# Kernel optimization log

Measured on AMD Instinct MI355X. Metric: run time of the kernel, lower is better.

## Reference

```python
import jax, jax.numpy as jnp
import numpy as np

N_NODES = 50000
N_EDGES = 400000
D_IN = 64
D_HID = 64
D_OUT = 64
NEG_SLOPE = 0.2   # GATConv LeakyReLU slope
BN_EPS = 1e-5


def _add_self_loops(row, col, N):
    loop = jnp.arange(N, dtype=row.dtype)
    return jnp.concatenate([row, loop]), jnp.concatenate([col, loop])


def _gcn_conv(x, row, col, N, W, b):
    # PyG GCNConv: add self loops, symmetric normalization, sum aggregate, bias
    r, c = _add_self_loops(row, col, N)
    deg = jax.ops.segment_sum(jnp.ones_like(r, dtype=x.dtype), c, num_segments=N)
    dis = jnp.where(deg > 0, deg ** -0.5, 0.0)
    norm = dis[r] * dis[c]                       # [E+N]
    h = x @ W                                    # [N, out]
    out = jax.ops.segment_sum(h[r] * norm[:, None], c, num_segments=N)
    return out + b


def _gat_conv(x, row, col, N, W, att_src, att_dst, b, concat):
    # PyG GATConv: per-edge attention with softmax over incoming edges
    H, C = att_src.shape
    r, c = _add_self_loops(row, col, N)
    h = (x @ W).reshape(N, H, C)
    a_src = jnp.einsum('nhc,hc->nh', h, att_src)
    a_dst = jnp.einsum('nhc,hc->nh', h, att_dst)
    e = jax.nn.leaky_relu(a_src[r] + a_dst[c], NEG_SLOPE)   # [E', H]
    m = jax.ops.segment_max(e, c, num_segments=N)           # stable softmax per target
    e = jnp.exp(e - m[c])
    denom = jax.ops.segment_sum(e, c, num_segments=N)
    alpha = e / denom[c]                                    # [E', H]
    out = jax.ops.segment_sum(h[r] * alpha[:, :, None], c, num_segments=N)  # [N,H,C]
    out = out.reshape(N, H * C) if concat else out.mean(axis=1)
    return out + b


def _sage_conv(x, row, col, N, Wl, bl, Wr):
    # PyG SAGEConv(aggr='mean', normalize=True): lin_l(mean_j x_j) + lin_r(x), then L2-normalize
    s = jax.ops.segment_sum(x[row], col, num_segments=N)
    cnt = jax.ops.segment_sum(jnp.ones_like(row, dtype=x.dtype), col, num_segments=N)
    mean = s / jnp.maximum(cnt, 1.0)[:, None]
    out = mean @ Wl + bl + x @ Wr
    n = jnp.linalg.norm(out, axis=-1, keepdims=True)
    return out / jnp.maximum(n, 1e-12)


def _forward(x, edge_index, gate_w1, gate_b1, gate_w2, gate_b2,
             gcn_w1, gcn_b1, bn_gamma, bn_beta, gcn_w2, gcn_b2,
             gat_w1, gat_att_src1, gat_att_dst1, gat_b1,
             gat_w2, gat_att_src2, gat_att_dst2, gat_b2,
             sage_wl1, sage_bl1, sage_wr1, sage_wl2, sage_bl2, sage_wr2):
    N = x.shape[0]
    row, col = edge_index[0], edge_index[1]
    # gate: mean node feature -> MLP -> softmax over 3 models
    g = jnp.mean(x, axis=0, keepdims=True)
    w = jax.nn.softmax(jax.nn.relu(g @ gate_w1 + gate_b1) @ gate_w2 + gate_b2, axis=-1)
    # GCN branch (eval: BatchNorm with running mean=0, var=1; dropout off)
    h = _gcn_conv(x, row, col, N, gcn_w1, gcn_b1)
    h = h * (bn_gamma / jnp.sqrt(1.0 + BN_EPS)) + bn_beta
    h = jax.nn.relu(h)
    out_gcn = _gcn_conv(h, row, col, N, gcn_w2, gcn_b2)
    # GAT branch: hidden layer 4 heads concat + ELU, output layer 1 head mean
    h = jax.nn.elu(_gat_conv(x, row, col, N, gat_w1, gat_att_src1, gat_att_dst1, gat_b1, True))
    out_gat = _gat_conv(h, row, col, N, gat_w2, gat_att_src2, gat_att_dst2, gat_b2, False)
    # SAGE branch
    h = jax.nn.relu(_sage_conv(x, row, col, N, sage_wl1, sage_bl1, sage_wr1))
    out_sage = _sage_conv(h, row, col, N, sage_wl2, sage_bl2, sage_wr2)
    return w[0, 0] * out_gcn + w[0, 1] * out_gat + w[0, 2] * out_sage


def setup_inputs() -> dict:
    key = jax.random.key(0)
    ks = jax.random.split(key, 16)
    def nrm(k, shape, scale=0.05):
        return jax.random.normal(k, shape, dtype=jnp.float32) * scale
    inp = {}
    inp['x'] = jax.random.normal(ks[0], (N_NODES, D_IN), dtype=jnp.float32)
    inp['edge_index'] = jax.random.randint(ks[1], (2, N_EDGES), 0, N_NODES, dtype=jnp.int32)
    inp['gate_w1'] = nrm(ks[2], (D_IN, 64)); inp['gate_b1'] = jnp.zeros((64,), jnp.float32)
    inp['gate_w2'] = nrm(ks[3], (64, 3));    inp['gate_b2'] = jnp.zeros((3,), jnp.float32)
    inp['gcn_w1'] = nrm(ks[4], (D_IN, D_HID)); inp['gcn_b1'] = jnp.zeros((D_HID,), jnp.float32)
    inp['bn_gamma'] = jnp.ones((D_HID,), jnp.float32); inp['bn_beta'] = jnp.zeros((D_HID,), jnp.float32)
    inp['gcn_w2'] = nrm(ks[5], (D_HID, D_OUT)); inp['gcn_b2'] = jnp.zeros((D_OUT,), jnp.float32)
    inp['gat_w1'] = nrm(ks[6], (D_IN, 4 * D_HID))
    inp['gat_att_src1'] = nrm(ks[7], (4, D_HID)); inp['gat_att_dst1'] = nrm(ks[8], (4, D_HID))
    inp['gat_b1'] = jnp.zeros((4 * D_HID,), jnp.float32)
    inp['gat_w2'] = nrm(ks[9], (4 * D_HID, D_OUT))
    inp['gat_att_src2'] = nrm(ks[10], (1, D_OUT)); inp['gat_att_dst2'] = nrm(ks[11], (1, D_OUT))
    inp['gat_b2'] = jnp.zeros((D_OUT,), jnp.float32)
    inp['sage_wl1'] = nrm(ks[12], (D_IN, D_HID)); inp['sage_bl1'] = jnp.zeros((D_HID,), jnp.float32)
    inp['sage_wr1'] = nrm(ks[13], (D_IN, D_HID))
    inp['sage_wl2'] = nrm(ks[14], (D_HID, D_OUT)); inp['sage_bl2'] = jnp.zeros((D_OUT,), jnp.float32)
    inp['sage_wr2'] = nrm(ks[15], (D_HID, D_OUT))
    return inp


def reference(x, edge_index, gate_w1, gate_b1, gate_w2, gate_b2,
              gcn_w1, gcn_b1, bn_gamma, bn_beta, gcn_w2, gcn_b2,
              gat_w1, gat_att_src1, gat_att_dst1, gat_b1,
              gat_w2, gat_att_src2, gat_att_dst2, gat_b2,
              sage_wl1, sage_bl1, sage_wr1, sage_wl2, sage_bl2, sage_wr2):
    return _forward(x, edge_index, gate_w1, gate_b1, gate_w2, gate_b2,
                    gcn_w1, gcn_b1, bn_gamma, bn_beta, gcn_w2, gcn_b2,
                    gat_w1, gat_att_src1, gat_att_dst1, gat_b1,
                    gat_w2, gat_att_src2, gat_att_dst2, gat_b2,
                    sage_wl1, sage_bl1, sage_wr1, sage_wl2, sage_bl2, sage_wr2)
```

## Files before the change

### kernel.cpp

```cpp
#include <hip/hip_runtime.h>
#include <hip/hip_bf16.h>
#include <math.h>

#define NN 50000
#define NE 400000

typedef __attribute__((ext_vector_type(8))) short bf16x8;
typedef __attribute__((ext_vector_type(4))) float f32x4;

__device__ __forceinline__ float lrelu(float v){ return v > 0.f ? v : 0.2f*v; }
__device__ __forceinline__ float elu1(float v){ return v > 0.f ? v : expm1f(v); }
__device__ __forceinline__ float bflo(unsigned int u){ return __uint_as_float(u << 16); }
__device__ __forceinline__ float bfhi(unsigned int u){ return __uint_as_float(u & 0xffff0000u); }
__device__ __forceinline__ unsigned short f2bf(float f){
  __hip_bfloat16 h = __float2bfloat16(f);
  return *(unsigned short*)&h;
}
__device__ __forceinline__ unsigned int pack2(float lo, float hi){
  return (unsigned int)f2bf(lo) | ((unsigned int)f2bf(hi) << 16);
}

__device__ __forceinline__ void stage_tab(unsigned short* Wt, const unsigned short* Wb, int tid){
  #pragma unroll
  for(int s = 0; s < 2; s++){
    int c = tid + s*256;
    int n = c >> 3, ko = (c & 7)*8;
    *(bf16x8*)&Wt[n*72 + ko] = *(const bf16x8*)&Wb[n*64 + ko];
  }
}

__global__ void k_count(const int* __restrict__ col, int* __restrict__ cnt, int E){
  int e = blockIdx.x*blockDim.x + threadIdx.x;
  if(e < E) atomicAdd(&cnt[col[e]], 1);
}

__global__ void k_alloc(const int* __restrict__ cnt, int* __restrict__ offs,
                        float* __restrict__ dis, float* __restrict__ invc,
                        int* __restrict__ total, int N){
  int i = blockIdx.x*blockDim.x + threadIdx.x;
  int lane = threadIdx.x & 63;
  int v = (i < N) ? cnt[i] : 0;
  int x = v;
  #pragma unroll
  for(int d = 1; d < 64; d <<= 1){ int t = __shfl_up(x, d, 64); if(lane >= d) x += t; }
  int base = 0;
  if(lane == 63 && x > 0) base = atomicAdd(total, x);
  base = __shfl(base, 63, 64);
  if(i < N){
    offs[i] = base + x - v;
    dis[i]  = 1.0f / sqrtf((float)(v + 1));
    invc[i] = 1.0f / fmaxf((float)v, 1.0f);
  }
}

__global__ void k_fill(const int* __restrict__ row, const int* __restrict__ col,
                       const int* __restrict__ offs, int* __restrict__ cursor,
                       int* __restrict__ csr, int E){
  int e = blockIdx.x*blockDim.x + threadIdx.x;
  if(e < E){
    int c = col[e];
    int pos = offs[c] + atomicAdd(&cursor[c], 1);
    csr[pos] = row[e];
  }
}

struct PKS { const float* src; unsigned short* dst; int kshift; int ldw; int col0; };
struct PKP { PKS s[11]; };

__global__ void k_packw(PKP p){
  PKS s = p.s[blockIdx.x];
  int K = 1 << s.kshift;
  int total = K << 6;
  for(int idx = threadIdx.x; idx < total; idx += 256){
    int n = idx >> s.kshift, k = idx & (K - 1);
    s.dst[idx] = f2bf(s.src[(size_t)k*s.ldw + s.col0 + n]);
  }
}

__global__ void k_castsum(const float* __restrict__ x, unsigned short* __restrict__ xb,
                          float* __restrict__ gsum, int N){
  __shared__ float part[4][64];
  int lane = threadIdx.x & 63, w = threadIdx.x >> 6;
  float s = 0.f;
  for(int r = blockIdx.x*4 + w; r < N; r += gridDim.x*4){
    float v = x[(size_t)r*64 + lane];
    xb[(size_t)r*64 + lane] = f2bf(v);
    s += v;
  }
  part[w][lane] = s;
  __syncthreads();
  if(w == 0) atomicAdd(&gsum[lane], part[0][lane]+part[1][lane]+part[2][lane]+part[3][lane]);
}

__global__ void k_gate(const float* __restrict__ gsum,
                       const float* __restrict__ w1, const float* __restrict__ b1,
                       const float* __restrict__ w2, const float* __restrict__ b2,
                       float* __restrict__ gatew){
  __shared__ float g[64]; __shared__ float hid[64]; __shared__ float lg[3];
  int t = threadIdx.x;
  g[t] = gsum[t] * (1.0f/(float)NN);
  __syncthreads();
  float acc = b1[t];
  for(int i = 0; i < 64; i++) acc += g[i]*w1[i*64 + t];
  hid[t] = fmaxf(acc, 0.f);
  __syncthreads();
  if(t < 3){
    float a = b2[t];
    for(int j = 0; j < 64; j++) a += hid[j]*w2[j*3 + t];
    lg[t] = a;
  }
  __syncthreads();
  if(t == 0){
    float m = fmaxf(lg[0], fmaxf(lg[1], lg[2]));
    float e0 = expf(lg[0]-m), e1 = expf(lg[1]-m), e2 = expf(lg[2]-m);
    float s = e0 + e1 + e2;
    gatew[0] = e0/s; gatew[1] = e1/s; gatew[2] = e2/s;
  }
}

__global__ void k_fold1(const float* __restrict__ w1, const float* __restrict__ as,
                        const float* __restrict__ ad, float* __restrict__ wsd){
  int t = threadIdx.x;
  int k = t & 63, h = t >> 6;
  float ssrc = 0.f, sdst = 0.f;
  for(int c = 0; c < 64; c++){
    float w = w1[k*256 + h*64 + c];
    ssrc += w * as[h*64 + c];
    sdst += w * ad[h*64 + c];
  }
  wsd[k*8 + h] = ssrc;
  wsd[k*8 + 4 + h] = sdst;
}

__global__ void k_attdotx(const unsigned short* __restrict__ xb, const float* __restrict__ wsd,
                          float* __restrict__ asrc, float* __restrict__ adst, int N){
  __shared__ float ws[64*8];
  int tid = threadIdx.x;
  ws[tid] = wsd[tid];
  ws[tid + 256] = wsd[tid + 256];
  __syncthreads();
  int node = blockIdx.x*16 + (tid >> 4);
  int l = tid & 15;
  if(node >= N) return;
  uint2 u = *(const uint2*)&xb[(size_t)node*64 + l*4];
  float v0 = bflo(u.x), v1 = bfhi(u.x), v2 = bflo(u.y), v3 = bfhi(u.y);
  float s[8];
  #pragma unroll
  for(int h = 0; h < 8; h++){
    s[h] = v0*ws[(l*4+0)*8+h] + v1*ws[(l*4+1)*8+h] + v2*ws[(l*4+2)*8+h] + v3*ws[(l*4+3)*8+h];
  }
  #pragma unroll
  for(int d = 8; d >= 1; d >>= 1){
    #pragma unroll
    for(int h = 0; h < 8; h++) s[h] += __shfl_xor(s[h], d, 16);
  }
  if(l == 0){
    float4 o1; o1.x = s[0]; o1.y = s[1]; o1.z = s[2]; o1.w = s[3];
    float4 o2; o2.x = s[4]; o2.y = s[5]; o2.z = s[6]; o2.w = s[7];
    *(float4*)&asrc[node*4] = o1;
    *(float4*)&adst[node*4] = o2;
  }
}

__global__ void k_edgew1(const float* __restrict__ asrc, const float* __restrict__ adst,
                         const int* __restrict__ offs, const int* __restrict__ cnt,
                         const int* __restrict__ csr,
                         float* __restrict__ wvE, float* __restrict__ rdenN,
                         float* __restrict__ wvS, int N){
  int node = blockIdx.x*4 + (threadIdx.x >> 6);
  int lane = threadIdx.x & 63;
  if(node >= N) return;
  float4 ad = *(const float4*)&adst[node*4];
  float a0 = 0.f, a1 = 0.f, a2 = 0.f, a3 = 0.f;
  int e0 = offs[node], e1 = e0 + cnt[node];
  for(int e = e0 + lane; e < e1; e += 64){
    int s = csr[e];
    float4 as = *(const float4*)&asrc[s*4];
    float4 w;
    w.x = expf(lrelu(as.x + ad.x));
    w.y = expf(lrelu(as.y + ad.y));
    w.z = expf(lrelu(as.z + ad.z));
    w.w = expf(lrelu(as.w + ad.w));
    a0 += w.x; a1 += w.y; a2 += w.z; a3 += w.w;
    *(float4*)&wvE[(size_t)e*4] = w;
  }
  #pragma unroll
  for(int d = 32; d >= 1; d >>= 1){
    a0 += __shfl_xor(a0, d, 64); a1 += __shfl_xor(a1, d, 64);
    a2 += __shfl_xor(a2, d, 64); a3 += __shfl_xor(a3, d, 64);
  }
  float4 asl = *(const float4*)&asrc[node*4];
  float4 ws;
  ws.x = expf(lrelu(asl.x + ad.x));
  ws.y = expf(lrelu(asl.y + ad.y));
  ws.z = expf(lrelu(asl.z + ad.z));
  ws.w = expf(lrelu(asl.w + ad.w));
  if(lane == 0){
    float4 rd;
    rd.x = 1.0f/(a0 + ws.x); rd.y = 1.0f/(a1 + ws.y);
    rd.z = 1.0f/(a2 + ws.z); rd.w = 1.0f/(a3 + ws.w);
    *(float4*)&rdenN[node*4] = rd;
    *(float4*)&wvS[node*4] = ws;
  }
}

__global__ void k_edgew2(const float* __restrict__ asrc, const float* __restrict__ adst,
                         const int* __restrict__ offs, const int* __restrict__ cnt,
                         const int* __restrict__ csr,
                         float* __restrict__ wvE, float* __restrict__ rdenN,
                         float* __restrict__ wvS, int N){
  int node = blockIdx.x*4 + (threadIdx.x >> 6);
  int lane = threadIdx.x & 63;
  if(node >= N) return;
  float ad = adst[node];
  float acc = 0.f;
  int e0 = offs[node], e1 = e0 + cnt[node];
  for(int e = e0 + lane; e < e1; e += 64){
    float w = expf(lrelu(asrc[csr[e]] + ad));
    acc += w;
    wvE[e] = w;
  }
  #pragma unroll
  for(int d = 32; d >= 1; d >>= 1) acc += __shfl_xor(acc, d, 64);
  float ws = expf(lrelu(asrc[node] + ad));
  if(lane == 0){
    rdenN[node] = 1.0f/(acc + ws);
    wvS[node] = ws;
  }
}

__global__ void k_aggx(const unsigned short* __restrict__ xb,
                       const float* __restrict__ wvE, const float* __restrict__ rden,
                       const float* __restrict__ wvS,
                       const float* __restrict__ dis, const float* __restrict__ invc,
                       const int* __restrict__ offs, const int* __restrict__ cnt,
                       const int* __restrict__ csr,
                       unsigned short* __restrict__ z, unsigned short* __restrict__ agcnx,
                       unsigned short* __restrict__ asagex, int N){
  int node = blockIdx.x*4 + (threadIdx.x >> 6);
  int lane = threadIdx.x & 63;
  if(node >= N) return;
  int half = lane >> 5, subl = lane & 31;
  float zg[4][2] = {{0,0},{0,0},{0,0},{0,0}};
  float gg[2] = {0,0}, ssv[2] = {0,0};
  int e0 = offs[node], e1 = e0 + cnt[node];
  #pragma unroll 2
  for(int e = e0 + half; e < e1; e += 2){
    int s = csr[e];
    float4 w4 = *(const float4*)&wvE[(size_t)e*4];
    float ds = dis[s];
    unsigned int u = *(const unsigned int*)&xb[(size_t)s*64 + subl*2];
    float xl = bflo(u), xh = bfhi(u);
    zg[0][0] = fmaf(w4.x, xl, zg[0][0]); zg[0][1] = fmaf(w4.x, xh, zg[0][1]);
    zg[1][0] = fmaf(w4.y, xl, zg[1][0]); zg[1][1] = fmaf(w4.y, xh, zg[1][1]);
    zg[2][0] = fmaf(w4.z, xl, zg[2][0]); zg[2][1] = fmaf(w4.z, xh, zg[2][1]);
    zg[3][0] = fmaf(w4.w, xl, zg[3][0]); zg[3][1] = fmaf(w4.w, xh, zg[3][1]);
    gg[0] = fmaf(ds, xl, gg[0]); gg[1] = fmaf(ds, xh, gg[1]);
    ssv[0] += xl; ssv[1] += xh;
  }
  #pragma unroll
  for(int h = 0; h < 4; h++){
    zg[h][0] += __shfl_xor(zg[h][0], 32, 64);
    zg[h][1] += __shfl_xor(zg[h][1], 32, 64);
  }
  gg[0] += __shfl_xor(gg[0], 32, 64); gg[1] += __shfl_xor(gg[1], 32, 64);
  ssv[0] += __shfl_xor(ssv[0], 32, 64); ssv[1] += __shfl_xor(ssv[1], 32, 64);
  if(half == 0){
    unsigned int un = *(const unsigned int*)&xb[(size_t)node*64 + subl*2];
    float xl = bflo(un), xh = bfhi(un);
    float4 ws4 = *(const float4*)&wvS[node*4];
    float4 rd4 = *(const float4*)&rden[node*4];
    unsigned int* zp = (unsigned int*)&z[(size_t)node*256 + subl*2];
    zp[0]   = pack2((zg[0][0] + ws4.x*xl)*rd4.x, (zg[0][1] + ws4.x*xh)*rd4.x);
    zp[32]  = pack2((zg[1][0] + ws4.y*xl)*rd4.y, (zg[1][1] + ws4.y*xh)*rd4.y);
    zp[64]  = pack2((zg[2][0] + ws4.z*xl)*rd4.z, (zg[2][1] + ws4.z*xh)*rd4.z);
    zp[96]  = pack2((zg[3][0] + ws4.w*xl)*rd4.w, (zg[3][1] + ws4.w*xh)*rd4.w);
    float dc = dis[node], ic = invc[node];
    *(unsigned int*)&agcnx[(size_t)node*64 + subl*2] =
        pack2(dc*fmaf(dc, xl, gg[0]), dc*fmaf(dc, xh, gg[1]));
    *(unsigned int*)&asagex[(size_t)node*64 + subl*2] = pack2(ssv[0]*ic, ssv[1]*ic);
  }
}

__global__ void k_aggf(const unsigned short* __restrict__ a1, const unsigned short* __restrict__ s1,
                       const unsigned short* __restrict__ h2,
                       const float* __restrict__ wvE, const float* __restrict__ rden,
                       const float* __restrict__ wvS,
                       const float* __restrict__ dis, const float* __restrict__ invc,
                       const int* __restrict__ offs, const int* __restrict__ cnt,
                       const int* __restrict__ csr,
                       unsigned short* __restrict__ A2agg, unsigned short* __restrict__ S2agg,
                       unsigned short* __restrict__ T2, int N){
  int node = blockIdx.x*4 + (threadIdx.x >> 6);
  int lane = threadIdx.x & 63;
  if(node >= N) return;
  int half = lane >> 5, subl = lane & 31;
  float aa[2] = {0,0}, ss[2] = {0,0}, tt[2] = {0,0};
  int e0 = offs[node], e1 = e0 + cnt[node];
  #pragma unroll 2
  for(int e = e0 + half; e < e1; e += 2){
    int s = csr[e];
    float ds = dis[s];
    float wv = wvE[e];
    unsigned int ua = *(const unsigned int*)&a1[(size_t)s*64 + subl*2];
    unsigned int us = *(const unsigned int*)&s1[(size_t)s*64 + subl*2];
    unsigned int uh = *(const unsigned int*)&h2[(size_t)s*64 + subl*2];
    aa[0] = fmaf(ds, bflo(ua), aa[0]); aa[1] = fmaf(ds, bfhi(ua), aa[1]);
    ss[0] += bflo(us); ss[1] += bfhi(us);
    tt[0] = fmaf(wv, bflo(uh), tt[0]); tt[1] = fmaf(wv, bfhi(uh), tt[1]);
  }
  aa[0] += __shfl_xor(aa[0], 32, 64); aa[1] += __shfl_xor(aa[1], 32, 64);
  ss[0] += __shfl_xor(ss[0], 32, 64); ss[1] += __shfl_xor(ss[1], 32, 64);
  tt[0] += __shfl_xor(tt[0], 32, 64); tt[1] += __shfl_xor(tt[1], 32, 64);
  if(half == 0){
    unsigned int uan = *(const unsigned int*)&a1[(size_t)node*64 + subl*2];
    unsigned int uhn = *(const unsigned int*)&h2[(size_t)node*64 + subl*2];
    float dc = dis[node], ic = invc[node];
    float rd = rden[node], wss = wvS[node];
    *(unsigned int*)&A2agg[(size_t)node*64 + subl*2] =
        pack2(dc*fmaf(dc, bflo(uan), aa[0]), dc*fmaf(dc, bfhi(uan), aa[1]));
    *(unsigned int*)&S2agg[(size_t)node*64 + subl*2] = pack2(ss[0]*ic, ss[1]*ic);
    *(unsigned int*)&T2[(size_t)node*64 + subl*2] =
        pack2(fmaf(wss, bflo(uhn), tt[0])*rd, fmaf(wss, bfhi(uhn), tt[1])*rd);
  }
}

struct MME {
  const unsigned short* A; const unsigned short* Wb;
  const unsigned short* A2; const unsigned short* Wb2;
  unsigned short* C;
  const float* b; const float* p1; const float* p2;
  int ep;
};
struct FSP {
  const unsigned short* z; const unsigned short* wb1; const float* b1;
  const unsigned short* wb2; const float* as2; const float* ad2;
  unsigned short* h2; float* asrc2; float* adst2;
  MME mm[2];
  int N;
};

__global__ __launch_bounds__(256, 4) void k_fused1(FSP p){
  __shared__ unsigned short smem[16896];
  const int N = p.N;
  int tid = threadIdx.x;
  int w = tid >> 6, lane = tid & 63, quad = lane >> 4, m16 = lane & 15;
  int rowa = blockIdx.x*64 + w*16 + m16;
  int rowc = rowa < N ? rowa : N - 1;
  int robase = blockIdx.x*64 + w*16 + quad*4;

  if(blockIdx.y == 0){
    unsigned short* GH = smem;
    int lr = w*16;
    #pragma unroll
    for(int h = 0; h < 4; h++){
      bf16x8 a0 = *(const bf16x8*)&p.z[(size_t)rowc*256 + h*64 + quad*8];
      bf16x8 a1 = *(const bf16x8*)&p.z[(size_t)rowc*256 + h*64 + 32 + quad*8];
      f32x4 acc[4];
      #pragma unroll
      for(int t = 0; t < 4; t++){ acc[t][0]=0.f; acc[t][1]=0.f; acc[t][2]=0.f; acc[t][3]=0.f; }
      #pragma unroll
      for(int t = 0; t < 4; t++){
        const unsigned short* wb = p.wb1 + (size_t)h*4096 + (t*16 + m16)*64;
        bf16x8 b0 = *(const bf16x8*)&wb[quad*8];
        bf16x8 b1v = *(const bf16x8*)&wb[32 + quad*8];
        acc[t] = __builtin_amdgcn_mfma_f32_16x16x32_bf16(a0, b0, acc[t], 0, 0, 0);
        acc[t] = __builtin_amdgcn_mfma_f32_16x16x32_bf16(a1, b1v, acc[t], 0, 0, 0);
      }
      #pragma unroll
      for(int t = 0; t < 4; t++){
        float bv = p.b1[h*64 + t*16 + m16];
        #pragma unroll
        for(int r = 0; r < 4; r++){
          GH[(lr + quad*4 + r)*264 + h*64 + t*16 + m16] = f2bf(elu1(acc[t][r] + bv));
        }
      }
    }
    __syncthreads();
    f32x4 acc2[4];
    #pragma unroll
    for(int t = 0; t < 4; t++){ acc2[t][0]=0.f; acc2[t][1]=0.f; acc2[t][2]=0.f; acc2[t][3]=0.f; }
    #pragma unroll
    for(int kc = 0; kc < 256; kc += 64){
      bf16x8 a0 = *(const bf16x8*)&GH[(lr + m16)*264 + kc + quad*8];
      bf16x8 a1 = *(const bf16x8*)&GH[(lr + m16)*264 + kc + 32 + quad*8];
      #pragma unroll
      for(int t = 0; t < 4; t++){
        const unsigned short* wb = p.wb2 + (size_t)(t*16 + m16)*256 + kc;
        bf16x8 b0 = *(const bf16x8*)&wb[quad*8];
        bf16x8 b1v = *(const bf16x8*)&wb[32 + quad*8];
        acc2[t] = __builtin_amdgcn_mfma_f32_16x16x32_bf16(a0, b0, acc2[t], 0, 0, 0);
        acc2[t] = __builtin_amdgcn_mfma_f32_16x16x32_bf16(a1, b1v, acc2[t], 0, 0, 0);
      }
    }
    #pragma unroll
    for(int t = 0; t < 4; t++){
      int col = t*16 + m16;
      #pragma unroll
      for(int r = 0; r < 4; r++){
        int ro = robase + r;
        if(ro < N) p.h2[(size_t)ro*64 + col] = f2bf(acc2[t][r]);
      }
    }
    float ps[4] = {0,0,0,0}, pd[4] = {0,0,0,0};
    #pragma unroll
// ... 151 lines not shown
  }
  float w0 = gatew[0], w1 = gatew[1], w2 = gatew[2];
  int robase = blockIdx.x*64 + w*16 + quad*4;
  float vs[4][4], n2[4] = {0,0,0,0};
  #pragma unroll
  for(int t = 0; t < 4; t++){
    float bsv = bl2[t*16 + m16];
    #pragma unroll
    for(int r = 0; r < 4; r++){ vs[t][r] = accs[t][r] + bsv; n2[r] = fmaf(vs[t][r], vs[t][r], n2[r]); }
  }
  #pragma unroll
  for(int d = 8; d >= 1; d >>= 1){
    #pragma unroll
    for(int r = 0; r < 4; r++) n2[r] += __shfl_xor(n2[r], d, 64);
  }
  float inv[4];
  #pragma unroll
  for(int r = 0; r < 4; r++) inv[r] = 1.0f / fmaxf(sqrtf(n2[r]), 1e-12f);
  #pragma unroll
  for(int t = 0; t < 4; t++){
    int col = t*16 + m16;
    float bg = gcn_b2[col], bt = gat_b2[col];
    #pragma unroll
    for(int r = 0; r < 4; r++){
      int ro = robase + r;
      if(ro < N){
        float t2 = bflo((unsigned int)T2[(size_t)ro*64 + col]);
        out[(size_t)ro*64 + col] = w0*(accg[t][r] + bg) + w1*(t2 + bt) + w2*vs[t][r]*inv[r];
      }
    }
  }
}

extern "C" void kernel_launch(void* const* d_in, const int* in_sizes, int n_in,
                              void* d_out, int out_size, void* d_ws, size_t ws_size,
                              hipStream_t stream){
  const float* x        = (const float*)d_in[0];
  const int*   ei       = (const int*)d_in[1];
  const int*   row      = ei;
  const int*   col      = ei + NE;
  const float* gate_w1  = (const float*)d_in[2];
  const float* gate_b1  = (const float*)d_in[3];
  const float* gate_w2  = (const float*)d_in[4];
  const float* gate_b2  = (const float*)d_in[5];
  const float* gcn_w1   = (const float*)d_in[6];
  const float* gcn_b1   = (const float*)d_in[7];
  const float* bn_gamma = (const float*)d_in[8];
  const float* bn_beta  = (const float*)d_in[9];
  const float* gcn_w2   = (const float*)d_in[10];
  const float* gcn_b2   = (const float*)d_in[11];
  const float* gat_w1   = (const float*)d_in[12];
  const float* gat_as1  = (const float*)d_in[13];
  const float* gat_ad1  = (const float*)d_in[14];
  const float* gat_b1   = (const float*)d_in[15];
  const float* gat_w2   = (const float*)d_in[16];
  const float* gat_as2  = (const float*)d_in[17];
  const float* gat_ad2  = (const float*)d_in[18];
  const float* gat_b2   = (const float*)d_in[19];
  const float* sage_wl1 = (const float*)d_in[20];
  const float* sage_bl1 = (const float*)d_in[21];
  const float* sage_wr1 = (const float*)d_in[22];
  const float* sage_wl2 = (const float*)d_in[23];
  const float* sage_bl2 = (const float*)d_in[24];
  const float* sage_wr2 = (const float*)d_in[25];
  float* out = (float*)d_out;

  char* wp = (char*)d_ws;
  auto alloc = [&](size_t bytes)->char*{ char* p = wp; wp += (bytes + 255) & ~(size_t)255; return p; };
  int*   cnt    = (int*)  alloc((size_t)NN*4);
  int*   cursor = (int*)  alloc((size_t)NN*4);
  float* gsum   = (float*)alloc(64*4);
  int*   total  = (int*)  alloc(256);
  size_t zbytes = (size_t)(wp - (char*)cnt);
  int*   offs   = (int*)  alloc((size_t)NN*4);
  int*   csr    = (int*)  alloc((size_t)NE*4);
  float* dis    = (float*)alloc((size_t)NN*4);
  float* invc   = (float*)alloc((size_t)NN*4);
  float* gatew  = (float*)alloc(16);
  float* wsd    = (float*)alloc(64*8*4);
  float* asrc1  = (float*)alloc((size_t)NN*4*4);
  float* adst1  = (float*)alloc((size_t)NN*4*4);
  float* asrc2  = (float*)alloc((size_t)NN*4);
  float* adst2  = (float*)alloc((size_t)NN*4);
  float* wvE1   = (float*)alloc((size_t)NE*4*4);
  float* rden1  = (float*)alloc((size_t)NN*4*4);
  float* wvS1   = (float*)alloc((size_t)NN*4*4);
  float* wvE2   = (float*)alloc((size_t)NE*4);
  float* rden2  = (float*)alloc((size_t)NN*4);
  float* wvS2   = (float*)alloc((size_t)NN*4);
  unsigned short* xb     = (unsigned short*)alloc((size_t)NN*64*2);
  unsigned short* z      = (unsigned short*)alloc((size_t)NN*256*2);
  unsigned short* agcnx  = (unsigned short*)alloc((size_t)NN*64*2);
  unsigned short* asagex = (unsigned short*)alloc((size_t)NN*64*2);
  unsigned short* a1     = (unsigned short*)alloc((size_t)NN*64*2);
  unsigned short* s1     = (unsigned short*)alloc((size_t)NN*64*2);
  unsigned short* h2     = (unsigned short*)alloc((size_t)NN*64*2);
  unsigned short* A2agg  = (unsigned short*)alloc((size_t)NN*64*2);
  unsigned short* S2agg  = (unsigned short*)alloc((size_t)NN*64*2);
  unsigned short* T2     = (unsigned short*)alloc((size_t)NN*64*2);
  unsigned short* wb_gcn1 = (unsigned short*)alloc((size_t)64*64*2);
  unsigned short* wb_wl1  = (unsigned short*)alloc((size_t)64*64*2);
  unsigned short* wb_wr1  = (unsigned short*)alloc((size_t)64*64*2);
  unsigned short* wb_gat1 = (unsigned short*)alloc((size_t)256*64*2);
  unsigned short* wb_gat2 = (unsigned short*)alloc((size_t)64*256*2);
  unsigned short* wb_gcn2 = (unsigned short*)alloc((size_t)64*64*2);
  unsigned short* wb_wl2  = (unsigned short*)alloc((size_t)64*64*2);
  unsigned short* wb_wr2  = (unsigned short*)alloc((size_t)64*64*2);

  hipMemsetAsync(cnt, 0, zbytes, stream);

  const int gN  = (NN + 63) / 64;
  const int g4  = NN / 4;
  const int g16 = NN / 16;
  const int gA  = (NN + 255) / 256;

  {
    PKP pk = {};
    pk.s[0]  = {gcn_w1,   wb_gcn1,            6, 64,  0};
    pk.s[1]  = {sage_wl1, wb_wl1,             6, 64,  0};
    pk.s[2]  = {sage_wr1, wb_wr1,             6, 64,  0};
    pk.s[3]  = {gat_w1,   wb_gat1 + 0*64*64,  6, 256, 0};
    pk.s[4]  = {gat_w1,   wb_gat1 + 1*64*64,  6, 256, 64};
    pk.s[5]  = {gat_w1,   wb_gat1 + 2*64*64,  6, 256, 128};
    pk.s[6]  = {gat_w1,   wb_gat1 + 3*64*64,  6, 256, 192};
    pk.s[7]  = {gat_w2,   wb_gat2,            8, 64,  0};
    pk.s[8]  = {gcn_w2,   wb_gcn2,            6, 64,  0};
    pk.s[9]  = {sage_wl2, wb_wl2,             6, 64,  0};
    pk.s[10] = {sage_wr2, wb_wr2,             6, 64,  0};
    k_packw<<<11, 256, 0, stream>>>(pk);
  }

  k_count<<<(NE+255)/256, 256, 0, stream>>>(col, cnt, NE);
  k_alloc<<<gA, 256, 0, stream>>>(cnt, offs, dis, invc, total, NN);
  k_fill <<<(NE+255)/256, 256, 0, stream>>>(row, col, offs, cursor, csr, NE);
  k_castsum<<<256, 256, 0, stream>>>(x, xb, gsum, NN);
  k_gate  <<<1, 64, 0, stream>>>(gsum, gate_w1, gate_b1, gate_w2, gate_b2, gatew);
  k_fold1 <<<1, 256, 0, stream>>>(gat_w1, gat_as1, gat_ad1, wsd);
  k_attdotx<<<g16, 256, 0, stream>>>(xb, wsd, asrc1, adst1, NN);
  k_edgew1<<<g4, 256, 0, stream>>>(asrc1, adst1, offs, cnt, csr, wvE1, rden1, wvS1, NN);

  k_aggx<<<g4, 256, 0, stream>>>(xb, wvE1, rden1, wvS1, dis, invc, offs, cnt, csr,
                                 z, agcnx, asagex, NN);

  {
    FSP p = {};
    p.N = NN;
    p.z = z; p.wb1 = wb_gat1; p.b1 = gat_b1;
    p.wb2 = wb_gat2; p.as2 = gat_as2; p.ad2 = gat_ad2;
    p.h2 = h2; p.asrc2 = asrc2; p.adst2 = adst2;
    p.mm[0] = {agcnx, wb_gcn1, nullptr, nullptr, a1, gcn_b1, bn_gamma, bn_beta, 1};
    p.mm[1] = {asagex, wb_wl1, xb, wb_wr1, s1, sage_bl1, nullptr, nullptr, 3};
    k_fused1<<<dim3(gN,3), 256, 0, stream>>>(p);
  }

  k_edgew2<<<g4, 256, 0, stream>>>(asrc2, adst2, offs, cnt, csr, wvE2, rden2, wvS2, NN);

  k_aggf<<<g4, 256, 0, stream>>>(a1, s1, h2, wvE2, rden2, wvS2, dis, invc,
                                 offs, cnt, csr, A2agg, S2agg, T2, NN);

  k_mm_final<<<gN, 256, 0, stream>>>(A2agg, wb_gcn2, gcn_b2, S2agg, wb_wl2, sage_bl2,
                                     s1, wb_wr2, T2, gat_b2, gatew, out, NN);
}
```

Baseline: 361.9 us.

## Fuse edge-weight kernels into aggregation and merge small prologue kernels

The separate edge-softmax kernels are removed for both GAT layers. Attention weights and the denominators are now recomputed inside the aggregation loops, so the per-edge weight arrays are no longer written to or read from memory. The small setup kernels (weight packing, degree count, cast/sum, attention fold, CSR fill, gate, attention dot) are merged into two launches that branch on block index. This cuts launch count and global traffic, at the cost of redundant exp work per feature lane.

```diff
diff --git a/kernel.cpp b/kernel.cpp
--- a/kernel.cpp
+++ b/kernel.cpp
@@ -29,9 +29,60 @@
   }
 }
 
-__global__ void k_count(const int* __restrict__ col, int* __restrict__ cnt, int E){
-  int e = blockIdx.x*blockDim.x + threadIdx.x;
-  if(e < E) atomicAdd(&cnt[col[e]], 1);
+struct PKS { const float* src; unsigned short* dst; int kshift; int ldw; int col0; };
+
+struct PreP {
+  PKS pk[11];
+  const int* col; int* cnt;
+  const float* x; unsigned short* xb; float* gsum;
+  const float* gw1; const float* gas; const float* gad; float* wsd;
+};
+
+#define NB_CNT ((NE+255)/256)
+
+__global__ __launch_bounds__(256) void k_pre(PreP p){
+  __shared__ float part[4][64];
+  int b = blockIdx.x, tid = threadIdx.x;
+  if(b < 11){
+    PKS s = p.pk[b];
+    int K = 1 << s.kshift;
+    int total = K << 6;
+    for(int idx = tid; idx < total; idx += 256){
+      int n = idx >> s.kshift, k = idx & (K - 1);
+      s.dst[idx] = f2bf(s.src[(size_t)k*s.ldw + s.col0 + n]);
+    }
+    return;
+  }
+  if(b < 11 + NB_CNT){
+    int e = (b - 11)*256 + tid;
+    if(e < NE) atomicAdd(&p.cnt[p.col[e]], 1);
+    return;
+  }
+  if(b < 11 + NB_CNT + 256){
+    int lb = b - (11 + NB_CNT);
+    int lane = tid & 63, w = tid >> 6;
+    float s = 0.f;
+    for(int r = lb*4 + w; r < NN; r += 256*4){
+      float v = p.x[(size_t)r*64 + lane];
+      p.xb[(size_t)r*64 + lane] = f2bf(v);
+      s += v;
+    }
+    part[w][lane] = s;
+    __syncthreads();
+    if(w == 0) atomicAdd(&p.gsum[lane], part[0][lane]+part[1][lane]+part[2][lane]+part[3][lane]);
+    return;
+  }
+  {
+    int k = tid & 63, h = tid >> 6;
+    float ssrc = 0.f, sdst = 0.f;
+    for(int c = 0; c < 64; c++){
+      float w = p.gw1[k*256 + h*64 + c];
+      ssrc += w * p.gas[h*64 + c];
+      sdst += w * p.gad[h*64 + c];
+    }
+    p.wsd[k*8 + h] = ssrc;
+    p.wsd[k*8 + 4 + h] = sdst;
+  }
 }
 
 __global__ void k_alloc(const int* __restrict__ cnt, int* __restrict__ offs,
@@ -53,96 +104,60 @@
   }
 }
 
-__global__ void k_fill(const int* __restrict__ row, const int* __restrict__ col,
-                       const int* __restrict__ offs, int* __restrict__ cursor,
-                       int* __restrict__ csr, int E){
-  int e = blockIdx.x*blockDim.x + threadIdx.x;
-  if(e < E){
-    int c = col[e];
-    int pos = offs[c] + atomicAdd(&cursor[c], 1);
-    csr[pos] = row[e];
-  }
-}
-
-struct PKS { const float* src; unsigned short* dst; int kshift; int ldw; int col0; };
-struct PKP { PKS s[11]; };
-
-__global__ void k_packw(PKP p){
-  PKS s = p.s[blockIdx.x];
-  int K = 1 << s.kshift;
-  int total = K << 6;
-  for(int idx = threadIdx.x; idx < total; idx += 256){
-    int n = idx >> s.kshift, k = idx & (K - 1);
-    s.dst[idx] = f2bf(s.src[(size_t)k*s.ldw + s.col0 + n]);
-  }
-}
-
-__global__ void k_castsum(const float* __restrict__ x, unsigned short* __restrict__ xb,
-                          float* __restrict__ gsum, int N){
-  __shared__ float part[4][64];
-  int lane = threadIdx.x & 63, w = threadIdx.x >> 6;
-  float s = 0.f;
-  for(int r = blockIdx.x*4 + w; r < N; r += gridDim.x*4){
-    float v = x[(size_t)r*64 + lane];
-    xb[(size_t)r*64 + lane] = f2bf(v);
-    s += v;
-  }
-  part[w][lane] = s;
+struct MidP {
+  const int* row; const int* col; const int* offs; int* cursor; int* csr;
+  const float* gsum; const float* w1; const float* b1; const float* w2; const float* b2;
+  float* gatew;
+  const unsigned short* xb; const float* wsd; float* asrc; float* adst;
+};
+
+#define NB_ATT (NN/16)
+
+__global__ __launch_bounds__(256) void k_mid(MidP p){
+  __shared__ float ws[64*8];
+  __shared__ float g[64]; __shared__ float hid[64]; __shared__ float lg[3];
+  int b = blockIdx.x, tid = threadIdx.x;
+  if(b < NB_CNT){
+    int e = b*256 + tid;
+    if(e < NE){
+      int c = p.col[e];
+      int pos = p.offs[c] + atomicAdd(&p.cursor[c], 1);
+      p.csr[pos] = p.row[e];
+    }
+    return;
+  }
+  if(b == NB_CNT){
+    int t = tid;
+    if(t < 64) g[t] = p.gsum[t] * (1.0f/(float)NN);
+    __syncthreads();
+    if(t < 64){
+      float acc = p.b1[t];
+      for(int i = 0; i < 64; i++) acc += g[i]*p.w1[i*64 + t];
+      hid[t] = fmaxf(acc, 0.f);
+    }
+    __syncthreads();
+    if(t < 3){
+      float a = p.b2[t];
+      for(int j = 0; j < 64; j++) a += hid[j]*p.w2[j*3 + t];
+      lg[t] = a;
+    }
+    __syncthreads();
+    if(t == 0){
+      float m = fmaxf(lg[0], fmaxf(lg[1], lg[2]));
+      float e0 = expf(lg[0]-m), e1 = expf(lg[1]-m), e2 = expf(lg[2]-m);
+      float s = e0 + e1 + e2;
+      p.gatew[0] = e0/s; p.gatew[1] = e1/s; p.gatew[2] = e2/s;
+    }
+    return;
+  }
+  int lb = b - (NB_CNT + 1);
+  ws[tid] = p.wsd[tid];
+  ws[tid + 256] = p.wsd[tid + 256];
   __syncthreads();
-  if(w == 0) atomicAdd(&gsum[lane], part[0][lane]+part[1][lane]+part[2][lane]+part[3][lane]);
-}
-
-__global__ void k_gate(const float* __restrict__ gsum,
-                       const float* __restrict__ w1, const float* __restrict__ b1,
-                       const float* __restrict__ w2, const float* __restrict__ b2,
-                       float* __restrict__ gatew){
-  __shared__ float g[64]; __shared__ float hid[64]; __shared__ float lg[3];
-  int t = threadIdx.x;
-  g[t] = gsum[t] * (1.0f/(float)NN);
-  __syncthreads();
-  float acc = b1[t];
-  for(int i = 0; i < 64; i++) acc += g[i]*w1[i*64 + t];
-  hid[t] = fmaxf(acc, 0.f);
-  __syncthreads();
-  if(t < 3){
-    float a = b2[t];
-    for(int j = 0; j < 64; j++) a += hid[j]*w2[j*3 + t];
-    lg[t] = a;
-  }
-  __syncthreads();
-  if(t == 0){
-    float m = fmaxf(lg[0], fmaxf(lg[1], lg[2]));
-    float e0 = expf(lg[0]-m), e1 = expf(lg[1]-m), e2 = expf(lg[2]-m);
-    float s = e0 + e1 + e2;
-    gatew[0] = e0/s; gatew[1] = e1/s; gatew[2] = e2/s;
-  }
-}
-
-__global__ void k_fold1(const float* __restrict__ w1, const float* __restrict__ as,
-                        const float* __restrict__ ad, float* __restrict__ wsd){
-  int t = threadIdx.x;
-  int k = t & 63, h = t >> 6;
-  float ssrc = 0.f, sdst = 0.f;
-  for(int c = 0; c < 64; c++){
-    float w = w1[k*256 + h*64 + c];
-    ssrc += w * as[h*64 + c];
-    sdst += w * ad[h*64 + c];
-  }
-  wsd[k*8 + h] = ssrc;
-  wsd[k*8 + 4 + h] = sdst;
-}
-
-__global__ void k_attdotx(const unsigned short* __restrict__ xb, const float* __restrict__ wsd,
-                          float* __restrict__ asrc, float* __restrict__ adst, int N){
-  __shared__ float ws[64*8];
-  int tid = threadIdx.x;
-  ws[tid] = wsd[tid];
-  ws[tid + 256] = wsd[tid + 256];
-  __syncthreads();
-  int node = blockIdx.x*16 + (tid >> 4);
+  int node = lb*16 + (tid >> 4);
   int l = tid & 15;
-  if(node >= N) return;
-  uint2 u = *(const uint2*)&xb[(size_t)node*64 + l*4];
+  if(node >= NN) return;
+  uint2 u = *(const uint2*)&p.xb[(size_t)node*64 + l*4];
   float v0 = bflo(u.x), v1 = bfhi(u.x), v2 = bflo(u.y), v3 = bfhi(u.y);
   float s[8];
   #pragma unroll
@@ -157,170 +172,119 @@
   if(l == 0){
     float4 o1; o1.x = s[0]; o1.y = s[1]; o1.z = s[2]; o1.w = s[3];
     float4 o2; o2.x = s[4]; o2.y = s[5]; o2.z = s[6]; o2.w = s[7];
-    *(float4*)&asrc[node*4] = o1;
-    *(float4*)&adst[node*4] = o2;
-  }
-}
-
-__global__ void k_edgew1(const float* __restrict__ asrc, const float* __restrict__ adst,
-                         const int* __restrict__ offs, const int* __restrict__ cnt,
-                         const int* __restrict__ csr,
-                         float* __restrict__ wvE, float* __restrict__ rdenN,
-                         float* __restrict__ wvS, int N){
+    *(float4*)&p.asrc[node*4] = o1;
+    *(float4*)&p.adst[node*4] = o2;
+  }
+}
+
+struct A1P {
+  const unsigned short* xb; const float* asrc1; const float* adst1;
+  const int* offs; const int* cnt; const int* csr;
+  const float* dis; const float* invc;
+  unsigned short* z; unsigned short* agcnx; unsigned short* asagex; int N;
+};
+
+__global__ void k_agg1(A1P p){
   int node = blockIdx.x*4 + (threadIdx.x >> 6);
   int lane = threadIdx.x & 63;
-  if(node >= N) return;
-  float4 ad = *(const float4*)&adst[node*4];
-  float a0 = 0.f, a1 = 0.f, a2 = 0.f, a3 = 0.f;
-  int e0 = offs[node], e1 = e0 + cnt[node];
-  for(int e = e0 + lane; e < e1; e += 64){
-    int s = csr[e];
-    float4 as = *(const float4*)&asrc[s*4];
-    float4 w;
-    w.x = expf(lrelu(as.x + ad.x));
-    w.y = expf(lrelu(as.y + ad.y));
-    w.z = expf(lrelu(as.z + ad.z));
-    w.w = expf(lrelu(as.w + ad.w));
-    a0 += w.x; a1 += w.y; a2 += w.z; a3 += w.w;
-    *(float4*)&wvE[(size_t)e*4] = w;
-  }
-  #pragma unroll
-  for(int d = 32; d >= 1; d >>= 1){
-    a0 += __shfl_xor(a0, d, 64); a1 += __shfl_xor(a1, d, 64);
-    a2 += __shfl_xor(a2, d, 64); a3 += __shfl_xor(a3, d, 64);
-  }
-  float4 asl = *(const float4*)&asrc[node*4];
-  float4 ws;
-  ws.x = expf(lrelu(asl.x + ad.x));
-  ws.y = expf(lrelu(asl.y + ad.y));
-  ws.z = expf(lrelu(asl.z + ad.z));
-  ws.w = expf(lrelu(asl.w + ad.w));
-  if(lane == 0){
-    float4 rd;
-    rd.x = 1.0f/(a0 + ws.x); rd.y = 1.0f/(a1 + ws.y);
-    rd.z = 1.0f/(a2 + ws.z); rd.w = 1.0f/(a3 + ws.w);
-    *(float4*)&rdenN[node*4] = rd;
-    *(float4*)&wvS[node*4] = ws;
-  }
-}
-
-__global__ void k_edgew2(const float* __restrict__ asrc, const float* __restrict__ adst,
-                         const int* __restrict__ offs, const int* __restrict__ cnt,
-                         const int* __restrict__ csr,
-                         float* __restrict__ wvE, float* __restrict__ rdenN,
-                         float* __restrict__ wvS, int N){
-  int node = blockIdx.x*4 + (threadIdx.x >> 6);
-  int lane = threadIdx.x & 63;
-  if(node >= N) return;
-  float ad = adst[node];
-  float acc = 0.f;
-  int e0 = offs[node], e1 = e0 + cnt[node];
-  for(int e = e0 + lane; e < e1; e += 64){
-    float w = expf(lrelu(asrc[csr[e]] + ad));
-    acc += w;
-    wvE[e] = w;
-  }
-  #pragma unroll
-  for(int d = 32; d >= 1; d >>= 1) acc += __shfl_xor(acc, d, 64);
-  float ws = expf(lrelu(asrc[node] + ad));
-  if(lane == 0){
-    rdenN[node] = 1.0f/(acc + ws);
-    wvS[node] = ws;
-  }
-}
-
-__global__ void k_aggx(const unsigned short* __restrict__ xb,
-                       const float* __restrict__ wvE, const float* __restrict__ rden,
-                       const float* __restrict__ wvS,
-                       const float* __restrict__ dis, const float* __restrict__ invc,
-                       const int* __restrict__ offs, const int* __restrict__ cnt,
-                       const int* __restrict__ csr,
-                       unsigned short* __restrict__ z, unsigned short* __restrict__ agcnx,
-                       unsigned short* __restrict__ asagex, int N){
-  int node = blockIdx.x*4 + (threadIdx.x >> 6);
-  int lane = threadIdx.x & 63;
-  if(node >= N) return;
+  if(node >= p.N) return;
   int half = lane >> 5, subl = lane & 31;
+  float4 ad4 = *(const float4*)&p.adst1[node*4];
   float zg[4][2] = {{0,0},{0,0},{0,0},{0,0}};
-  float gg[2] = {0,0}, ssv[2] = {0,0};
-  int e0 = offs[node], e1 = e0 + cnt[node];
+  float gg[2] = {0,0}, ssv[2] = {0,0}, wsum[4] = {0,0,0,0};
+  int e0 = p.offs[node], e1 = e0 + p.cnt[node];
   #pragma unroll 2
   for(int e = e0 + half; e < e1; e += 2){
-    int s = csr[e];
-    float4 w4 = *(const float4*)&wvE[(size_t)e*4];
-    float ds = dis[s];
-    unsigned int u = *(const unsigned int*)&xb[(size_t)s*64 + subl*2];
+    int s = p.csr[e];
+    float4 as4 = *(const float4*)&p.asrc1[s*4];
+    float ds = p.dis[s];
+    unsigned int u = *(const unsigned int*)&p.xb[(size_t)s*64 + subl*2];
+    float w0 = expf(lrelu(as4.x + ad4.x));
+    float w1 = expf(lrelu(as4.y + ad4.y));
+    float w2 = expf(lrelu(as4.z + ad4.z));
+    float w3 = expf(lrelu(as4.w + ad4.w));
     float xl = bflo(u), xh = bfhi(u);
-    zg[0][0] = fmaf(w4.x, xl, zg[0][0]); zg[0][1] = fmaf(w4.x, xh, zg[0][1]);
-    zg[1][0] = fmaf(w4.y, xl, zg[1][0]); zg[1][1] = fmaf(w4.y, xh, zg[1][1]);
-    zg[2][0] = fmaf(w4.z, xl, zg[2][0]); zg[2][1] = fmaf(w4.z, xh, zg[2][1]);
-    zg[3][0] = fmaf(w4.w, xl, zg[3][0]); zg[3][1] = fmaf(w4.w, xh, zg[3][1]);
+    zg[0][0] = fmaf(w0, xl, zg[0][0]); zg[0][1] = fmaf(w0, xh, zg[0][1]);
+    zg[1][0] = fmaf(w1, xl, zg[1][0]); zg[1][1] = fmaf(w1, xh, zg[1][1]);
+    zg[2][0] = fmaf(w2, xl, zg[2][0]); zg[2][1] = fmaf(w2, xh, zg[2][1]);
+    zg[3][0] = fmaf(w3, xl, zg[3][0]); zg[3][1] = fmaf(w3, xh, zg[3][1]);
     gg[0] = fmaf(ds, xl, gg[0]); gg[1] = fmaf(ds, xh, gg[1]);
     ssv[0] += xl; ssv[1] += xh;
+    wsum[0] += w0; wsum[1] += w1; wsum[2] += w2; wsum[3] += w3;
   }
   #pragma unroll
   for(int h = 0; h < 4; h++){
     zg[h][0] += __shfl_xor(zg[h][0], 32, 64);
     zg[h][1] += __shfl_xor(zg[h][1], 32, 64);
+    wsum[h]  += __shfl_xor(wsum[h], 32, 64);
   }
   gg[0] += __shfl_xor(gg[0], 32, 64); gg[1] += __shfl_xor(gg[1], 32, 64);
   ssv[0] += __shfl_xor(ssv[0], 32, 64); ssv[1] += __shfl_xor(ssv[1], 32, 64);
   if(half == 0){
-    unsigned int un = *(const unsigned int*)&xb[(size_t)node*64 + subl*2];
+    unsigned int un = *(const unsigned int*)&p.xb[(size_t)node*64 + subl*2];
     float xl = bflo(un), xh = bfhi(un);
-    float4 ws4 = *(const float4*)&wvS[node*4];
-    float4 rd4 = *(const float4*)&rden[node*4];
-    unsigned int* zp = (unsigned int*)&z[(size_t)node*256 + subl*2];
-    zp[0]   = pack2((zg[0][0] + ws4.x*xl)*rd4.x, (zg[0][1] + ws4.x*xh)*rd4.x);
-    zp[32]  = pack2((zg[1][0] + ws4.y*xl)*rd4.y, (zg[1][1] + ws4.y*xh)*rd4.y);
-    zp[64]  = pack2((zg[2][0] + ws4.z*xl)*rd4.z, (zg[2][1] + ws4.z*xh)*rd4.z);
-    zp[96]  = pack2((zg[3][0] + ws4.w*xl)*rd4.w, (zg[3][1] + ws4.w*xh)*rd4.w);
-    float dc = dis[node], ic = invc[node];
-    *(unsigned int*)&agcnx[(size_t)node*64 + subl*2] =
+    float4 asn = *(const float4*)&p.asrc1[node*4];
+    float s0 = expf(lrelu(asn.x + ad4.x));
+    float s1v = expf(lrelu(asn.y + ad4.y));
+    float s2 = expf(lrelu(asn.z + ad4.z));
+    float s3 = expf(lrelu(asn.w + ad4.w));
+    float rd0 = 1.0f/(wsum[0] + s0), rd1 = 1.0f/(wsum[1] + s1v);
+    float rd2 = 1.0f/(wsum[2] + s2), rd3 = 1.0f/(wsum[3] + s3);
+    unsigned int* zp = (unsigned int*)&p.z[(size_t)node*256 + subl*2];
+    zp[0]  = pack2((zg[0][0] + s0*xl)*rd0,  (zg[0][1] + s0*xh)*rd0);
+    zp[32] = pack2((zg[1][0] + s1v*xl)*rd1, (zg[1][1] + s1v*xh)*rd1);
+    zp[64] = pack2((zg[2][0] + s2*xl)*rd2,  (zg[2][1] + s2*xh)*rd2);
+    zp[96] = pack2((zg[3][0] + s3*xl)*rd3,  (zg[3][1] + s3*xh)*rd3);
+    float dc = p.dis[node], ic = p.invc[node];
+    *(unsigned int*)&p.agcnx[(size_t)node*64 + subl*2] =
         pack2(dc*fmaf(dc, xl, gg[0]), dc*fmaf(dc, xh, gg[1]));
-    *(unsigned int*)&asagex[(size_t)node*64 + subl*2] = pack2(ssv[0]*ic, ssv[1]*ic);
-  }
-}
-
-__global__ void k_aggf(const unsigned short* __restrict__ a1, const unsigned short* __restrict__ s1,
-                       const unsigned short* __restrict__ h2,
-                       const float* __restrict__ wvE, const float* __restrict__ rden,
-                       const float* __restrict__ wvS,
-                       const float* __restrict__ dis, const float* __restrict__ invc,
-                       const int* __restrict__ offs, const int* __restrict__ cnt,
-                       const int* __restrict__ csr,
-                       unsigned short* __restrict__ A2agg, unsigned short* __restrict__ S2agg,
-                       unsigned short* __restrict__ T2, int N){
+    *(unsigned int*)&p.asagex[(size_t)node*64 + subl*2] = pack2(ssv[0]*ic, ssv[1]*ic);
+  }
+}
+
+struct A2P {
+  const unsigned short* a1; const unsigned short* s1; const unsigned short* h2;
+  const float* asrc2; const float* adst2;
+  const int* offs; const int* cnt; const int* csr;
+  const float* dis; const float* invc;
+  unsigned short* A2agg; unsigned short* S2agg; unsigned short* T2; int N;
+};
+
+__global__ void k_agg2(A2P p){
   int node = blockIdx.x*4 + (threadIdx.x >> 6);
   int lane = threadIdx.x & 63;
-  if(node >= N) return;
+  if(node >= p.N) return;
   int half = lane >> 5, subl = lane & 31;
-  float aa[2] = {0,0}, ss[2] = {0,0}, tt[2] = {0,0};
-  int e0 = offs[node], e1 = e0 + cnt[node];
+  float ad = p.adst2[node];
+  float aa[2] = {0,0}, ss[2] = {0,0}, tt[2] = {0,0}, wsum = 0.f;
+  int e0 = p.offs[node], e1 = e0 + p.cnt[node];
   #pragma unroll 2
   for(int e = e0 + half; e < e1; e += 2){
-    int s = csr[e];
-    float ds = dis[s];
-    float wv = wvE[e];
-    unsigned int ua = *(const unsigned int*)&a1[(size_t)s*64 + subl*2];
-    unsigned int us = *(const unsigned int*)&s1[(size_t)s*64 + subl*2];
-    unsigned int uh = *(const unsigned int*)&h2[(size_t)s*64 + subl*2];
+    int s = p.csr[e];
+    float wv = expf(lrelu(p.asrc2[s] + ad));
+    float ds = p.dis[s];
+    unsigned int ua = *(const unsigned int*)&p.a1[(size_t)s*64 + subl*2];
+    unsigned int us = *(const unsigned int*)&p.s1[(size_t)s*64 + subl*2];
+    unsigned int uh = *(const unsigned int*)&p.h2[(size_t)s*64 + subl*2];
     aa[0] = fmaf(ds, bflo(ua), aa[0]); aa[1] = fmaf(ds, bfhi(ua), aa[1]);
     ss[0] += bflo(us); ss[1] += bfhi(us);
     tt[0] = fmaf(wv, bflo(uh), tt[0]); tt[1] = fmaf(wv, bfhi(uh), tt[1]);
+    wsum += wv;
   }
   aa[0] += __shfl_xor(aa[0], 32, 64); aa[1] += __shfl_xor(aa[1], 32, 64);
   ss[0] += __shfl_xor(ss[0], 32, 64); ss[1] += __shfl_xor(ss[1], 32, 64);
   tt[0] += __shfl_xor(tt[0], 32, 64); tt[1] += __shfl_xor(tt[1], 32, 64);
+  wsum  += __shfl_xor(wsum, 32, 64);
   if(half == 0){
-    unsigned int uan = *(const unsigned int*)&a1[(size_t)node*64 + subl*2];
-    unsigned int uhn = *(const unsigned int*)&h2[(size_t)node*64 + subl*2];
-    float dc = dis[node], ic = invc[node];
-    float rd = rden[node], wss = wvS[node];
-    *(unsigned int*)&A2agg[(size_t)node*64 + subl*2] =
+    float wss = expf(lrelu(p.asrc2[node] + ad));
+    float rd = 1.0f/(wsum + wss);
+    unsigned int uan = *(const unsigned int*)&p.a1[(size_t)node*64 + subl*2];
+    unsigned int uhn = *(const unsigned int*)&p.h2[(size_t)node*64 + subl*2];
+    float dc = p.dis[node], ic = p.invc[node];
+    *(unsigned int*)&p.A2agg[(size_t)node*64 + subl*2] =
         pack2(dc*fmaf(dc, bflo(uan), aa[0]), dc*fmaf(dc, bfhi(uan), aa[1]));
-    *(unsigned int*)&S2agg[(size_t)node*64 + subl*2] = pack2(ss[0]*ic, ss[1]*ic);
-    *(unsigned int*)&T2[(size_t)node*64 + subl*2] =
+    *(unsigned int*)&p.S2agg[(size_t)node*64 + subl*2] = pack2(ss[0]*ic, ss[1]*ic);
+    *(unsigned int*)&p.T2[(size_t)node*64 + subl*2] =
         pack2(fmaf(wss, bflo(uhn), tt[0])*rd, fmaf(wss, bfhi(uhn), tt[1])*rd);
   }
 }
@@ -638,12 +602,6 @@
   float* adst1  = (float*)alloc((size_t)NN*4*4);
   float* asrc2  = (float*)alloc((size_t)NN*4);
   float* adst2  = (float*)alloc((size_t)NN*4);
-  float* wvE1   = (float*)alloc((size_t)NE*4*4);
-  float* rden1  = (float*)alloc((size_t)NN*4*4);
-  float* wvS1   = (float*)alloc((size_t)NN*4*4);
-  float* wvE2   = (float*)alloc((size_t)NE*4);
-  float* rden2  = (float*)alloc((size_t)NN*4);
-  float* wvS2   = (float*)alloc((size_t)NN*4);
   unsigned short* xb     = (unsigned short*)alloc((size_t)NN*64*2);
   unsigned short* z      = (unsigned short*)alloc((size_t)NN*256*2);
   unsigned short* agcnx  = (unsigned short*)alloc((size_t)NN*64*2);
@@ -667,36 +625,45 @@
 
   const int gN  = (NN + 63) / 64;
   const int g4  = NN / 4;
-  const int g16 = NN / 16;
   const int gA  = (NN + 255) / 256;
 
   {
-    PKP pk = {};
-    pk.s[0]  = {gcn_w1,   wb_gcn1,            6, 64,  0};
-    pk.s[1]  = {sage_wl1, wb_wl1,             6, 64,  0};
-    pk.s[2]  = {sage_wr1, wb_wr1,             6, 64,  0};
-    pk.s[3]  = {gat_w1,   wb_gat1 + 0*64*64,  6, 256, 0};
-    pk.s[4]  = {gat_w1,   wb_gat1 + 1*64*64,  6, 256, 64};
-    pk.s[5]  = {gat_w1,   wb_gat1 + 2*64*64,  6, 256, 128};
-    pk.s[6]  = {gat_w1,   wb_gat1 + 3*64*64,  6, 256, 192};
-    pk.s[7]  = {gat_w2,   wb_gat2,            8, 64,  0};
-    pk.s[8]  = {gcn_w2,   wb_gcn2,            6, 64,  0};
-    pk.s[9]  = {sage_wl2, wb_wl2,             6, 64,  0};
-    pk.s[10] = {sage_wr2, wb_wr2,             6, 64,  0};
-    k_packw<<<11, 256, 0, stream>>>(pk);
-  }
-
-  k_count<<<(NE+255)/256, 256, 0, stream>>>(col, cnt, NE);
+    PreP p = {};
+    p.pk[0]  = {gcn_w1,   wb_gcn1,            6, 64,  0};
+    p.pk[1]  = {sage_wl1, wb_wl1,             6, 64,  0};
+    p.pk[2]  = {sage_wr1, wb_wr1,             6, 64,  0};
+    p.pk[3]  = {gat_w1,   wb_gat1 + 0*64*64,  6, 256, 0};
+    p.pk[4]  = {gat_w1,   wb_gat1 + 1*64*64,  6, 256, 64};
+    p.pk[5]  = {gat_w1,   wb_gat1 + 2*64*64,  6, 256, 128};
+    p.pk[6]  = {gat_w1,   wb_gat1 + 3*64*64,  6, 256, 192};
+    p.pk[7]  = {gat_w2,   wb_gat2,            8, 64,  0};
+    p.pk[8]  = {gcn_w2,   wb_gcn2,            6, 64,  0};
+    p.pk[9]  = {sage_wl2, wb_wl2,             6, 64,  0};
+    p.pk[10] = {sage_wr2, wb_wr2,             6, 64,  0};
+    p.col = col; p.cnt = cnt;
+    p.x = x; p.xb = xb; p.gsum = gsum;
+    p.gw1 = gat_w1; p.gas = gat_as1; p.gad = gat_ad1; p.wsd = wsd;
+    k_pre<<<11 + NB_CNT + 256 + 1, 256, 0, stream>>>(p);
+  }
+
   k_alloc<<<gA, 256, 0, stream>>>(cnt, offs, dis, invc, total, NN);
-  k_fill <<<(NE+255)/256, 256, 0, stream>>>(row, col, offs, cursor, csr, NE);
-  k_castsum<<<256, 256, 0, stream>>>(x, xb, gsum, NN);
-  k_gate  <<<1, 64, 0, stream>>>(gsum, gate_w1, gate_b1, gate_w2, gate_b2, gatew);
-  k_fold1 <<<1, 256, 0, stream>>>(gat_w1, gat_as1, gat_ad1, wsd);
-  k_attdotx<<<g16, 256, 0, stream>>>(xb, wsd, asrc1, adst1, NN);
-  k_edgew1<<<g4, 256, 0, stream>>>(asrc1, adst1, offs, cnt, csr, wvE1, rden1, wvS1, NN);
-
-  k_aggx<<<g4, 256, 0, stream>>>(xb, wvE1, rden1, wvS1, dis, invc, offs, cnt, csr,
-                                 z, agcnx, asagex, NN);
+
+  {
+    MidP p = {};
+    p.row = row; p.col = col; p.offs = offs; p.cursor = cursor; p.csr = csr;
+    p.gsum = gsum; p.w1 = gate_w1; p.b1 = gate_b1; p.w2 = gate_w2; p.b2 = gate_b2;
+    p.gatew = gatew;
+    p.xb = xb; p.wsd = wsd; p.asrc = asrc1; p.adst = adst1;
+    k_mid<<<NB_CNT + 1 + NB_ATT, 256, 0, stream>>>(p);
+  }
+
+  {
+    A1P p = {};
+    p.xb = xb; p.asrc1 = asrc1; p.adst1 = adst1;
+    p.offs = offs; p.cnt = cnt; p.csr = csr; p.dis = dis; p.invc = invc;
+    p.z = z; p.agcnx = agcnx; p.asagex = asagex; p.N = NN;
+    k_agg1<<<g4, 256, 0, stream>>>(p);
+  }
 
   {
     FSP p = {};
@@ -709,10 +676,13 @@
     k_fused1<<<dim3(gN,3), 256, 0, stream>>>(p);
   }
 
-  k_edgew2<<<g4, 256, 0, stream>>>(asrc2, adst2, offs, cnt, csr, wvE2, rden2, wvS2, NN);
-
-  k_aggf<<<g4, 256, 0, stream>>>(a1, s1, h2, wvE2, rden2, wvS2, dis, invc,
-                                 offs, cnt, csr, A2agg, S2agg, T2, NN);
+  {
+    A2P p = {};
+    p.a1 = a1; p.s1 = s1; p.h2 = h2; p.asrc2 = asrc2; p.adst2 = adst2;
+    p.offs = offs; p.cnt = cnt; p.csr = csr; p.dis = dis; p.invc = invc;
+    p.A2agg = A2agg; p.S2agg = S2agg; p.T2 = T2; p.N = NN;
+    k_agg2<<<g4, 256, 0, stream>>>(p);
+  }
 
   k_mm_final<<<gN, 256, 0, stream>>>(A2agg, wb_gcn2, gcn_b2, S2agg, wb_wl2, sage_bl2,
                                      s1, wb_wr2, T2, gat_b2, gatew, out, NN);
```

Result: faster. 323.1 us (-10.7%).
